# Performance work log

Measured on AMD Instinct MI355X. Metric: run time of the kernel, lower is better.

The kernel has to match this reference:

```python
import jax, jax.numpy as jnp
import numpy as np

N_NODES = 100000
N_EDGES = 200000
B_GRAPHS = 128
H = 8
DC = 256
DE = 124           # dim_embedding; node features are DE + 4 = 128
DV = 64


def setup_inputs() -> dict:
    key = jax.random.key(0)
    ks = jax.random.split(key, 10)

    def unif(k, shape):
        stdv = 1.0 / np.sqrt(shape[-1])
        return jax.random.uniform(k, shape, jnp.float32, -stdv, stdv)

    x = jax.random.normal(ks[0], (N_NODES, DE + 4), jnp.float32)
    edge_index = jax.random.randint(ks[1], (2, N_EDGES), 0, N_NODES)
    batch = jnp.sort(jax.random.randint(ks[2], (N_NODES,), 0, B_GRAPHS))
    context = jax.random.normal(ks[3], (B_GRAPHS, DC), jnp.float32)
    Wq = unif(ks[4], (H, DC, DV))
    Wk = unif(ks[5], (H, DE + 4, DV))
    Wv = unif(ks[6], (H, DE + 4, DV))
    query_coef = unif(ks[7], (1,))
    Wf = unif(ks[8], (DV, DE))
    return {"x": x, "edge_index": edge_index, "batch": batch, "context": context,
            "Wq": Wq, "Wk": Wk, "Wv": Wv, "query_coef": query_coef, "Wf": Wf}


def reference(x, edge_index, batch, context, Wq, Wk, Wv, query_coef, Wf):
    # edge_index is unused by the original forward.
    n_heads, _, dv = Wq.shape
    n_graphs = context.shape[0]

    query = jnp.einsum('bc,hcv->hbv', context, Wq)       # [H, B, Dv]
    keys = jnp.einsum('ne,hev->hnv', x, Wk)              # [H, N, Dv]
    values = jnp.einsum('ne,hev->hnv', x, Wv)            # [H, N, Dv]

    # original builds u = keys @ query^T [H,N,B] then gathers u[h,n,batch[n]];
    # compute only the gathered per-node score directly (same math).
    q_node = query[:, batch, :]                          # [H, N, Dv]
    u = jnp.sum(keys * q_node, axis=-1) / jnp.sqrt(jnp.asarray(dv, x.dtype))  # [H, N]

    # segment softmax per head over nodes of each graph
    seg_max = jax.vmap(lambda s: jax.ops.segment_max(s, batch, num_segments=n_graphs))(u)
    e = jnp.exp(u - seg_max[:, batch])                   # [H, N]
    seg_sum = jax.vmap(lambda s: jax.ops.segment_sum(s, batch, num_segments=n_graphs))(e)
    a = e / (seg_sum[:, batch] + 1e-16)                  # [H, N]

    v = a[..., None] * values                            # [H, N, Dv]
    agg = jax.vmap(lambda s: jax.ops.segment_sum(s, batch, num_segments=n_graphs))(v)  # [H, B, Dv]

    h = query_coef * query + agg                         # [H, B, Dv]
    h = jnp.einsum('hbv,ve->hbe', h, Wf)                 # [H, B, De]
    return jnp.sum(h, axis=0)                            # [B, De]
```

## Files before the change

### kernel.cpp

```cpp
#include <hip/hip_runtime.h>

#define N_NODES 100000
#define B_GRAPHS 128
#define H_HEADS 8
#define DC 256
#define DF 128
#define DV 64
#define DE 124
#define SPLITS 8
#define PART_STRIDE (H_HEADS * DF + H_HEADS)


__device__ __forceinline__ float red32(float v) {
  v += __int_as_float(__builtin_amdgcn_update_dpp(0, __float_as_int(v), 0xB1,  0xF, 0xF, true));
  v += __int_as_float(__builtin_amdgcn_update_dpp(0, __float_as_int(v), 0x4E,  0xF, 0xF, true));
  v += __int_as_float(__builtin_amdgcn_update_dpp(0, __float_as_int(v), 0x141, 0xF, 0xF, true));
  v += __int_as_float(__builtin_amdgcn_update_dpp(0, __float_as_int(v), 0x140, 0xF, 0xF, true));
  v += __int_as_float(__builtin_amdgcn_ds_swizzle(__float_as_int(v), 0x401f));
  return v;
}

__global__ __launch_bounds__(256) void k_prep(
    const float* __restrict__ context, const float* __restrict__ Wq,
    const float* __restrict__ Wk, const int* __restrict__ batch,
    float* __restrict__ query_ws, float* __restrict__ kq_ws, int* __restrict__ starts)
{
  const int b = blockIdx.x;
  const int t = threadIdx.x;
  __shared__ float ctxs[DC];
  __shared__ float qs[H_HEADS * DV];
  ctxs[t] = context[b * DC + t];
  if (t == 0) {
    int lo = 0, hi = N_NODES;
    while (lo < hi) { int m = (lo + hi) >> 1; if (batch[m] < b) lo = m + 1; else hi = m; }
    starts[b] = lo;
    if (b == 0) starts[B_GRAPHS] = N_NODES;
  }
  __syncthreads();
  for (int i = t; i < H_HEADS * DV; i += 256) {
    const int h = i >> 6, v = i & 63;
    const float* wq = Wq + (size_t)h * DC * DV + v;
    float acc = 0.f;
    for (int c = 0; c < DC; ++c) acc += ctxs[c] * wq[c * DV];
    qs[i] = acc;
    query_ws[(h * B_GRAPHS + b) * DV + v] = acc;
  }
  __syncthreads();
  for (int i = t; i < H_HEADS * DF; i += 256) {
    const int h = i >> 7, e = i & 127;
    const float4* wk = reinterpret_cast<const float4*>(Wk + ((size_t)h * DF + e) * DV);
    const float4* q4 = reinterpret_cast<const float4*>(qs + h * DV);
    float acc = 0.f;
    #pragma unroll
    for (int v4 = 0; v4 < DV / 4; ++v4) {
      const float4 a = wk[v4], q = q4[v4];
      acc += a.x * q.x + a.y * q.y + a.z * q.z + a.w * q.w;
    }
    kq_ws[(h * B_GRAPHS + b) * DF + e] = acc * 0.125f;
  }
}

__global__ __launch_bounds__(256) void k_main(
    const float* __restrict__ x, const float* __restrict__ kq_ws,
    const int* __restrict__ starts, float* __restrict__ partials)
{
  const int bid = blockIdx.x;
  const int g = bid >> 3, sp = bid & 7;
  const int t = threadIdx.x;
  const int grp = t >> 5, l32 = t & 31;
  const int s0 = starts[g], s1 = starts[g + 1];
  const int len = s1 - s0;
  const int i0 = s0 + (len * sp) / SPLITS;
  const int i1 = s0 + (len * (sp + 1)) / SPLITS;

  float4 kqr[H_HEADS];
  #pragma unroll
  for (int h = 0; h < H_HEADS; ++h)
    kqr[h] = *reinterpret_cast<const float4*>(kq_ws + (h * B_GRAPHS + g) * DF + 4 * l32);

  float4 s[H_HEADS];
  float l[H_HEADS];
  #pragma unroll
  for (int h = 0; h < H_HEADS; ++h) { s[h] = make_float4(0.f, 0.f, 0.f, 0.f); l[h] = 0.f; }

  int n = i0 + grp;
  float4 x4 = make_float4(0.f, 0.f, 0.f, 0.f);
  if (n < i1) x4 = *reinterpret_cast<const float4*>(x + (size_t)n * DF + 4 * l32);
  while (n < i1) {
    const int nn = n + 8;
    float4 xn = make_float4(0.f, 0.f, 0.f, 0.f);
    if (nn < i1) xn = *reinterpret_cast<const float4*>(x + (size_t)nn * DF + 4 * l32);
    float u[H_HEADS];
    #pragma unroll
    for (int h = 0; h < H_HEADS; ++h)
      u[h] = x4.x * kqr[h].x + x4.y * kqr[h].y + x4.z * kqr[h].z + x4.w * kqr[h].w;
    #pragma unroll
    for (int h = 0; h < H_HEADS; ++h) u[h] = red32(u[h]);
    #pragma unroll
    for (int h = 0; h < H_HEADS; ++h) {
      const float e = __expf(u[h]);
      l[h] += e;
      s[h].x += e * x4.x; s[h].y += e * x4.y; s[h].z += e * x4.z; s[h].w += e * x4.w;
    }
    x4 = xn; n = nn;
  }

  __shared__ float sbuf[8][H_HEADS][DF];
  __shared__ float lbuf[8][H_HEADS];
  #pragma unroll
  for (int h = 0; h < H_HEADS; ++h)
    *reinterpret_cast<float4*>(&sbuf[grp][h][4 * l32]) = s[h];
  if (l32 == 0) {
    #pragma unroll
    for (int h = 0; h < H_HEADS; ++h) lbuf[grp][h] = l[h];
  }
  __syncthreads();
  float* part = partials + (size_t)bid * PART_STRIDE;
  for (int i = t; i < H_HEADS * DF; i += 256) {
    const int h = i >> 7, e = i & 127;
    float acc = 0.f;
    #pragma unroll
    for (int gq = 0; gq < 8; ++gq) acc += sbuf[gq][h][e];
    part[i] = acc;
  }
  if (t < H_HEADS) {
    float acc = 0.f;
    #pragma unroll
    for (int gq = 0; gq < 8; ++gq) acc += lbuf[gq][t];
    part[H_HEADS * DF + t] = acc;
  }
}

__global__ __launch_bounds__(256) void k_final(
    const float* __restrict__ partials, const float* __restrict__ query_ws,
    const float* __restrict__ Wv, const float* __restrict__ Wf,
    const float* __restrict__ qcoef, float* __restrict__ out)
{
  const int g = blockIdx.x;
  const int t = threadIdx.x;
  __shared__ float w[H_HEADS][DF];
  __shared__ float lg[H_HEADS];
  __shared__ float Gp[4][DV];
  const float* part = partials + (size_t)g * SPLITS * PART_STRIDE;
  if (t < H_HEADS) {
    float acc = 0.f;
    for (int sp = 0; sp < SPLITS; ++sp) acc += part[sp * PART_STRIDE + H_HEADS * DF + t];
    lg[t] = acc;
  }
  __syncthreads();
  for (int i = t; i < H_HEADS * DF; i += 256) {
    float acc = 0.f;
    for (int sp = 0; sp < SPLITS; ++sp) acc += part[sp * PART_STRIDE + i];
    const int h = i >> 7;
    w[h][i & 127] = acc / (lg[h] + 1e-16f);
  }
  __syncthreads();
  const float qc = qcoef[0];
  const int v = t & 63, p = t >> 6;
  float acc = qc * (query_ws[((2 * p) * B_GRAPHS + g) * DV + v] +
                    query_ws[((2 * p + 1) * B_GRAPHS + g) * DV + v]);
  #pragma unroll
  for (int hh = 2 * p; hh <= 2 * p + 1; ++hh) {
    const float* wv = Wv + ((size_t)hh * DF) * DV + v;
    for (int e = 0; e < DF; ++e) acc += w[hh][e] * wv[e * DV];
  }
  Gp[p][v] = acc;
  __syncthreads();
  if (t < DE) {
    float o = 0.f;
    for (int v2 = 0; v2 < DV; ++v2) {
      const float Gv = Gp[0][v2] + Gp[1][v2] + Gp[2][v2] + Gp[3][v2];
      o += Gv * Wf[v2 * DE + t];
    }
    out[g * DE + t] = o;
  }
}

extern "C" void kernel_launch(void* const* d_in, const int* in_sizes, int n_in,
                              void* d_out, int out_size, void* d_ws, size_t ws_size,
                              hipStream_t stream) {
  const float* x       = (const float*)d_in[0];
  const int*   batch   = (const int*)d_in[2];
  const float* context = (const float*)d_in[3];
  const float* Wq      = (const float*)d_in[4];
  const float* Wk      = (const float*)d_in[5];
  const float* Wv      = (const float*)d_in[6];
  const float* qc      = (const float*)d_in[7];
  const float* Wf      = (const float*)d_in[8];
  float* out = (float*)d_out;

  float* ws       = (float*)d_ws;
  float* query_ws = ws;
  float* kq_ws    = ws + 65536;
  float* partials = ws + 196608;
  int*   starts   = (int*)(ws + 196608 + B_GRAPHS * SPLITS * PART_STRIDE);

  hipLaunchKernelGGL(k_prep, dim3(B_GRAPHS), dim3(256), 0, stream,
                     context, Wq, Wk, batch, query_ws, kq_ws, starts);
  hipLaunchKernelGGL(k_main, dim3(B_GRAPHS * SPLITS), dim3(256), 0, stream,
                     x, kq_ws, starts, partials);
  hipLaunchKernelGGL(k_final, dim3(B_GRAPHS), dim3(256), 0, stream,
                     partials, query_ws, Wv, Wf, qc, out);
}
```

Before: 148.0 us.

## Fuse final reduction into main kernel via last-block atomic counter

Drops the separate k_final launch. The last of the eight split blocks for each graph, detected with a threadfence and an atomic counter, now does the cross-split reduction and the Wv/Wf projection, reusing the shared buffers. It also vectorizes the query projection in k_prep with float4 loads over 128 threads. This saves one kernel launch and its gap. In exchange, some blocks run a serial tail, and correctness now depends on the counter being reset in k_prep.

```diff
diff --git a/kernel.cpp b/kernel.cpp
--- a/kernel.cpp
+++ b/kernel.cpp
@@ -23,7 +23,8 @@
 __global__ __launch_bounds__(256) void k_prep(
     const float* __restrict__ context, const float* __restrict__ Wq,
     const float* __restrict__ Wk, const int* __restrict__ batch,
-    float* __restrict__ query_ws, float* __restrict__ kq_ws, int* __restrict__ starts)
+    float* __restrict__ query_ws, float* __restrict__ kq_ws,
+    int* __restrict__ starts, int* __restrict__ cnt)
 {
   const int b = blockIdx.x;
   const int t = threadIdx.x;
@@ -34,16 +35,21 @@
     int lo = 0, hi = N_NODES;
     while (lo < hi) { int m = (lo + hi) >> 1; if (batch[m] < b) lo = m + 1; else hi = m; }
     starts[b] = lo;
+    cnt[b] = 0;
     if (b == 0) starts[B_GRAPHS] = N_NODES;
   }
   __syncthreads();
-  for (int i = t; i < H_HEADS * DV; i += 256) {
-    const int h = i >> 6, v = i & 63;
-    const float* wq = Wq + (size_t)h * DC * DV + v;
-    float acc = 0.f;
-    for (int c = 0; c < DC; ++c) acc += ctxs[c] * wq[c * DV];
-    qs[i] = acc;
-    query_ws[(h * B_GRAPHS + b) * DV + v] = acc;
+  if (t < H_HEADS * DV / 4) {
+    const int h = t >> 4, v4 = (t & 15) * 4;
+    const float4* wq = reinterpret_cast<const float4*>(Wq + (size_t)h * DC * DV + v4);
+    float4 acc = make_float4(0.f, 0.f, 0.f, 0.f);
+    for (int c = 0; c < DC; ++c) {
+      const float4 w = wq[c * (DV / 4)];
+      const float cc = ctxs[c];
+      acc.x += cc * w.x; acc.y += cc * w.y; acc.z += cc * w.z; acc.w += cc * w.w;
+    }
+    *reinterpret_cast<float4*>(qs + h * DV + v4) = acc;
+    *reinterpret_cast<float4*>(query_ws + (h * B_GRAPHS + b) * DV + v4) = acc;
   }
   __syncthreads();
   for (int i = t; i < H_HEADS * DF; i += 256) {
@@ -62,7 +68,11 @@
 
 __global__ __launch_bounds__(256) void k_main(
     const float* __restrict__ x, const float* __restrict__ kq_ws,
-    const int* __restrict__ starts, float* __restrict__ partials)
+    const int* __restrict__ starts, float* __restrict__ partials,
+    int* __restrict__ cnt,
+    const float* __restrict__ query_ws, const float* __restrict__ Wv,
+    const float* __restrict__ Wf, const float* __restrict__ qcoef,
+    float* __restrict__ out)
 {
   const int bid = blockIdx.x;
   const int g = bid >> 3, sp = bid & 7;
@@ -107,6 +117,7 @@
 
   __shared__ float sbuf[8][H_HEADS][DF];
   __shared__ float lbuf[8][H_HEADS];
+  __shared__ int amlast;
   #pragma unroll
   for (int h = 0; h < H_HEADS; ++h)
     *reinterpret_cast<float4*>(&sbuf[grp][h][4 * l32]) = s[h];
@@ -129,30 +140,27 @@
     for (int gq = 0; gq < 8; ++gq) acc += lbuf[gq][t];
     part[H_HEADS * DF + t] = acc;
   }
-}
-
-__global__ __launch_bounds__(256) void k_final(
-    const float* __restrict__ partials, const float* __restrict__ query_ws,
-    const float* __restrict__ Wv, const float* __restrict__ Wf,
-    const float* __restrict__ qcoef, float* __restrict__ out)
-{
-  const int g = blockIdx.x;
-  const int t = threadIdx.x;
-  __shared__ float w[H_HEADS][DF];
-  __shared__ float lg[H_HEADS];
-  __shared__ float Gp[4][DV];
-  const float* part = partials + (size_t)g * SPLITS * PART_STRIDE;
+
+  __threadfence();
+  if (t == 0) amlast = (atomicAdd(&cnt[g], 1) == SPLITS - 1) ? 1 : 0;
+  __syncthreads();
+  if (!amlast) return;
+  __threadfence();
+
+  float* w  = &sbuf[0][0][0];
+  float* Gp = &sbuf[2][0][0];
+  float* lg = &lbuf[0][0];
+  const float* pg = partials + (size_t)g * SPLITS * PART_STRIDE;
   if (t < H_HEADS) {
     float acc = 0.f;
-    for (int sp = 0; sp < SPLITS; ++sp) acc += part[sp * PART_STRIDE + H_HEADS * DF + t];
+    for (int spx = 0; spx < SPLITS; ++spx) acc += pg[spx * PART_STRIDE + H_HEADS * DF + t];
     lg[t] = acc;
   }
   __syncthreads();
   for (int i = t; i < H_HEADS * DF; i += 256) {
     float acc = 0.f;
-    for (int sp = 0; sp < SPLITS; ++sp) acc += part[sp * PART_STRIDE + i];
-    const int h = i >> 7;
-    w[h][i & 127] = acc / (lg[h] + 1e-16f);
+    for (int spx = 0; spx < SPLITS; ++spx) acc += pg[spx * PART_STRIDE + i];
+    w[i] = acc / (lg[i >> 7] + 1e-16f);
   }
   __syncthreads();
   const float qc = qcoef[0];
@@ -162,14 +170,15 @@
   #pragma unroll
   for (int hh = 2 * p; hh <= 2 * p + 1; ++hh) {
     const float* wv = Wv + ((size_t)hh * DF) * DV + v;
-    for (int e = 0; e < DF; ++e) acc += w[hh][e] * wv[e * DV];
-  }
-  Gp[p][v] = acc;
+    const float* wh = w + hh * DF;
+    for (int e = 0; e < DF; ++e) acc += wh[e] * wv[e * DV];
+  }
+  Gp[p * DV + v] = acc;
   __syncthreads();
   if (t < DE) {
     float o = 0.f;
     for (int v2 = 0; v2 < DV; ++v2) {
-      const float Gv = Gp[0][v2] + Gp[1][v2] + Gp[2][v2] + Gp[3][v2];
+      const float Gv = Gp[0 * DV + v2] + Gp[1 * DV + v2] + Gp[2 * DV + v2] + Gp[3 * DV + v2];
       o += Gv * Wf[v2 * DE + t];
     }
     out[g * DE + t] = o;
@@ -194,11 +203,10 @@
   float* kq_ws    = ws + 65536;
   float* partials = ws + 196608;
   int*   starts   = (int*)(ws + 196608 + B_GRAPHS * SPLITS * PART_STRIDE);
+  int*   cnt      = starts + B_GRAPHS + 1;
 
   hipLaunchKernelGGL(k_prep, dim3(B_GRAPHS), dim3(256), 0, stream,
-                     context, Wq, Wk, batch, query_ws, kq_ws, starts);
+                     context, Wq, Wk, batch, query_ws, kq_ws, starts, cnt);
   hipLaunchKernelGGL(k_main, dim3(B_GRAPHS * SPLITS), dim3(256), 0, stream,
-                     x, kq_ws, starts, partials);
-  hipLaunchKernelGGL(k_final, dim3(B_GRAPHS), dim3(256), 0, stream,
-                     partials, query_ws, Wv, Wf, qc, out);
-}
+                     x, kq_ws, starts, partials, cnt, query_ws, Wv, Wf, qc, out);
+}
```

Result: slower. 275.0 us (+85.8%).

## Fuse prep, main and final kernels into one per-graph kernel

Applied to the files above, without the earlier changes.

Merges the three launches into a single kernel with one 512-thread block per graph. Each block does its own binary search, query and key-query projection, node streaming and final projection, with shared-memory reduction replacing the global partials buffer. The node loop now prefetches two rows ahead across 16 warp groups. The cost is parallelism: only 128 blocks stream the 51 MB of x instead of 1024, which may underuse the GPU's memory bandwidth.

```diff
diff --git a/kernel.cpp b/kernel.cpp
--- a/kernel.cpp
+++ b/kernel.cpp
@@ -7,9 +7,8 @@
 #define DF 128
 #define DV 64
 #define DE 124
-#define SPLITS 8
-#define PART_STRIDE (H_HEADS * DF + H_HEADS)
-
+#define THREADS 512
+#define GROUPS 16
 
 __device__ __forceinline__ float red32(float v) {
   v += __int_as_float(__builtin_amdgcn_update_dpp(0, __float_as_int(v), 0xB1,  0xF, 0xF, true));
@@ -20,35 +19,49 @@
   return v;
 }
 
-__global__ __launch_bounds__(256) void k_prep(
+__global__ __launch_bounds__(THREADS) void k_all(
+    const float* __restrict__ x, const int* __restrict__ batch,
     const float* __restrict__ context, const float* __restrict__ Wq,
-    const float* __restrict__ Wk, const int* __restrict__ batch,
-    float* __restrict__ query_ws, float* __restrict__ kq_ws, int* __restrict__ starts)
+    const float* __restrict__ Wk, const float* __restrict__ Wv,
+    const float* __restrict__ qcoef, const float* __restrict__ Wf,
+    float* __restrict__ out)
 {
-  const int b = blockIdx.x;
+  const int g = blockIdx.x;
   const int t = threadIdx.x;
+
   __shared__ float ctxs[DC];
   __shared__ float qs[H_HEADS * DV];
-  ctxs[t] = context[b * DC + t];
-  if (t == 0) {
+  __shared__ float kqs[H_HEADS * DF];
+  __shared__ float sbuf[8][H_HEADS * DF];
+  __shared__ float lbuf[GROUPS][H_HEADS];
+  __shared__ float lg[H_HEADS];
+  __shared__ float wbuf[H_HEADS * DF];
+  __shared__ float Gpart[H_HEADS][DV];
+  __shared__ float Gv[DV];
+  __shared__ int srange[2];
+
+  if (t < 2) {
+    const int target = g + t;
     int lo = 0, hi = N_NODES;
-    while (lo < hi) { int m = (lo + hi) >> 1; if (batch[m] < b) lo = m + 1; else hi = m; }
-    starts[b] = lo;
-    if (b == 0) starts[B_GRAPHS] = N_NODES;
+    while (lo < hi) { int m = (lo + hi) >> 1; if (batch[m] < target) lo = m + 1; else hi = m; }
+    srange[t] = lo;
+  }
+  if (t < DC) ctxs[t] = context[g * DC + t];
+  __syncthreads();
+
+  {
+    const int h = t >> 6, v = t & 63;
+    const float* wq = Wq + (size_t)h * DC * DV + v;
+    float acc = 0.f;
+    #pragma unroll 4
+    for (int c = 0; c < DC; ++c) acc += ctxs[c] * wq[(size_t)c * DV];
+    qs[t] = acc;
   }
   __syncthreads();
-  for (int i = t; i < H_HEADS * DV; i += 256) {
-    const int h = i >> 6, v = i & 63;
-    const float* wq = Wq + (size_t)h * DC * DV + v;
-    float acc = 0.f;
-    for (int c = 0; c < DC; ++c) acc += ctxs[c] * wq[c * DV];
-    qs[i] = acc;
-    query_ws[(h * B_GRAPHS + b) * DV + v] = acc;
-  }
-  __syncthreads();
-  for (int i = t; i < H_HEADS * DF; i += 256) {
-    const int h = i >> 7, e = i & 127;
-    const float4* wk = reinterpret_cast<const float4*>(Wk + ((size_t)h * DF + e) * DV);
+
+  for (int i = t; i < H_HEADS * DF; i += THREADS) {
+    const int h = i >> 7;
+    const float4* wk = reinterpret_cast<const float4*>(Wk + (size_t)i * DV);
     const float4* q4 = reinterpret_cast<const float4*>(qs + h * DV);
     float acc = 0.f;
     #pragma unroll
@@ -56,122 +69,112 @@
       const float4 a = wk[v4], q = q4[v4];
       acc += a.x * q.x + a.y * q.y + a.z * q.z + a.w * q.w;
     }
-    kq_ws[(h * B_GRAPHS + b) * DF + e] = acc * 0.125f;
+    kqs[i] = acc * 0.125f;
   }
-}
+  __syncthreads();
 
-__global__ __launch_bounds__(256) void k_main(
-    const float* __restrict__ x, const float* __restrict__ kq_ws,
-    const int* __restrict__ starts, float* __restrict__ partials)
-{
-  const int bid = blockIdx.x;
-  const int g = bid >> 3, sp = bid & 7;
-  const int t = threadIdx.x;
   const int grp = t >> 5, l32 = t & 31;
-  const int s0 = starts[g], s1 = starts[g + 1];
-  const int len = s1 - s0;
-  const int i0 = s0 + (len * sp) / SPLITS;
-  const int i1 = s0 + (len * (sp + 1)) / SPLITS;
+  const int i0f = srange[0], i1 = srange[1];
 
   float4 kqr[H_HEADS];
   #pragma unroll
   for (int h = 0; h < H_HEADS; ++h)
-    kqr[h] = *reinterpret_cast<const float4*>(kq_ws + (h * B_GRAPHS + g) * DF + 4 * l32);
+    kqr[h] = *reinterpret_cast<const float4*>(kqs + h * DF + 4 * l32);
 
   float4 s[H_HEADS];
   float l[H_HEADS];
   #pragma unroll
   for (int h = 0; h < H_HEADS; ++h) { s[h] = make_float4(0.f, 0.f, 0.f, 0.f); l[h] = 0.f; }
 
-  int n = i0 + grp;
-  float4 x4 = make_float4(0.f, 0.f, 0.f, 0.f);
-  if (n < i1) x4 = *reinterpret_cast<const float4*>(x + (size_t)n * DF + 4 * l32);
+  int n = i0f + grp;
+  float4 a0 = make_float4(0.f, 0.f, 0.f, 0.f);
+  float4 a1 = make_float4(0.f, 0.f, 0.f, 0.f);
+  if (n < i1)          a0 = *reinterpret_cast<const float4*>(x + (size_t)n * DF + 4 * l32);
+  if (n + GROUPS < i1) a1 = *reinterpret_cast<const float4*>(x + (size_t)(n + GROUPS) * DF + 4 * l32);
   while (n < i1) {
-    const int nn = n + 8;
-    float4 xn = make_float4(0.f, 0.f, 0.f, 0.f);
-    if (nn < i1) xn = *reinterpret_cast<const float4*>(x + (size_t)nn * DF + 4 * l32);
+    float4 a2 = make_float4(0.f, 0.f, 0.f, 0.f);
+    if (n + 2 * GROUPS < i1)
+      a2 = *reinterpret_cast<const float4*>(x + (size_t)(n + 2 * GROUPS) * DF + 4 * l32);
     float u[H_HEADS];
     #pragma unroll
     for (int h = 0; h < H_HEADS; ++h)
-      u[h] = x4.x * kqr[h].x + x4.y * kqr[h].y + x4.z * kqr[h].z + x4.w * kqr[h].w;
+      u[h] = a0.x * kqr[h].x + a0.y * kqr[h].y + a0.z * kqr[h].z + a0.w * kqr[h].w;
     #pragma unroll
     for (int h = 0; h < H_HEADS; ++h) u[h] = red32(u[h]);
     #pragma unroll
     for (int h = 0; h < H_HEADS; ++h) {
       const float e = __expf(u[h]);
       l[h] += e;
-      s[h].x += e * x4.x; s[h].y += e * x4.y; s[h].z += e * x4.z; s[h].w += e * x4.w;
+      s[h].x += e * a0.x; s[h].y += e * a0.y; s[h].z += e * a0.z; s[h].w += e * a0.w;
     }
-    x4 = xn; n = nn;
+    a0 = a1; a1 = a2; n += GROUPS;
   }
 
-  __shared__ float sbuf[8][H_HEADS][DF];
-  __shared__ float lbuf[8][H_HEADS];
-  #pragma unroll
-  for (int h = 0; h < H_HEADS; ++h)
-    *reinterpret_cast<float4*>(&sbuf[grp][h][4 * l32]) = s[h];
-  if (l32 == 0) {
+  if (grp >= 8) {
     #pragma unroll
-    for (int h = 0; h < H_HEADS; ++h) lbuf[grp][h] = l[h];
+    for (int h = 0; h < H_HEADS; ++h)
+      *reinterpret_cast<float4*>(&sbuf[grp - 8][h * DF + 4 * l32]) = s[h];
+    if (l32 == 0) {
+      #pragma unroll
+      for (int h = 0; h < H_HEADS; ++h) lbuf[grp][h] = l[h];
+    }
   }
   __syncthreads();
-  float* part = partials + (size_t)bid * PART_STRIDE;
-  for (int i = t; i < H_HEADS * DF; i += 256) {
-    const int h = i >> 7, e = i & 127;
-    float acc = 0.f;
+  if (grp < 8) {
     #pragma unroll
-    for (int gq = 0; gq < 8; ++gq) acc += sbuf[gq][h][e];
-    part[i] = acc;
+    for (int h = 0; h < H_HEADS; ++h) {
+      const float4 o = *reinterpret_cast<const float4*>(&sbuf[grp][h * DF + 4 * l32]);
+      s[h].x += o.x; s[h].y += o.y; s[h].z += o.z; s[h].w += o.w;
+      l[h] += lbuf[grp + 8][h];
+    }
   }
+  __syncthreads();
+  if (grp < 8) {
+    #pragma unroll
+    for (int h = 0; h < H_HEADS; ++h)
+      *reinterpret_cast<float4*>(&sbuf[grp][h * DF + 4 * l32]) = s[h];
+    if (l32 == 0) {
+      #pragma unroll
+      for (int h = 0; h < H_HEADS; ++h) lbuf[grp][h] = l[h];
+    }
+  }
+  __syncthreads();
   if (t < H_HEADS) {
     float acc = 0.f;
     #pragma unroll
-    for (int gq = 0; gq < 8; ++gq) acc += lbuf[gq][t];
-    part[H_HEADS * DF + t] = acc;
-  }
-}
-
-__global__ __launch_bounds__(256) void k_final(
-    const float* __restrict__ partials, const float* __restrict__ query_ws,
-    const float* __restrict__ Wv, const float* __restrict__ Wf,
-    const float* __restrict__ qcoef, float* __restrict__ out)
-{
-  const int g = blockIdx.x;
-  const int t = threadIdx.x;
-  __shared__ float w[H_HEADS][DF];
-  __shared__ float lg[H_HEADS];
-  __shared__ float Gp[4][DV];
-  const float* part = partials + (size_t)g * SPLITS * PART_STRIDE;
-  if (t < H_HEADS) {
-    float acc = 0.f;
-    for (int sp = 0; sp < SPLITS; ++sp) acc += part[sp * PART_STRIDE + H_HEADS * DF + t];
+    for (int g8 = 0; g8 < 8; ++g8) acc += lbuf[g8][t];
     lg[t] = acc;
   }
   __syncthreads();
-  for (int i = t; i < H_HEADS * DF; i += 256) {
+  for (int i = t; i < H_HEADS * DF; i += THREADS) {
     float acc = 0.f;
-    for (int sp = 0; sp < SPLITS; ++sp) acc += part[sp * PART_STRIDE + i];
-    const int h = i >> 7;
-    w[h][i & 127] = acc / (lg[h] + 1e-16f);
+    #pragma unroll
+    for (int g8 = 0; g8 < 8; ++g8) acc += sbuf[g8][i];
+    wbuf[i] = acc / (lg[i >> 7] + 1e-16f);
   }
   __syncthreads();
+
   const float qc = qcoef[0];
-  const int v = t & 63, p = t >> 6;
-  float acc = qc * (query_ws[((2 * p) * B_GRAPHS + g) * DV + v] +
-                    query_ws[((2 * p + 1) * B_GRAPHS + g) * DV + v]);
-  #pragma unroll
-  for (int hh = 2 * p; hh <= 2 * p + 1; ++hh) {
-    const float* wv = Wv + ((size_t)hh * DF) * DV + v;
-    for (int e = 0; e < DF; ++e) acc += w[hh][e] * wv[e * DV];
+  {
+    const int h = t >> 6, v = t & 63;
+    const float* wv = Wv + (size_t)h * DF * DV + v;
+    const float* wh = wbuf + h * DF;
+    float acc = qc * qs[h * DV + v];
+    #pragma unroll 4
+    for (int e = 0; e < DF; ++e) acc += wh[e] * wv[(size_t)e * DV];
+    Gpart[h][v] = acc;
   }
-  Gp[p][v] = acc;
+  __syncthreads();
+  if (t < DV) {
+    float acc = 0.f;
+    #pragma unroll
+    for (int h = 0; h < H_HEADS; ++h) acc += Gpart[h][t];
+    Gv[t] = acc;
+  }
   __syncthreads();
   if (t < DE) {
     float o = 0.f;
-    for (int v2 = 0; v2 < DV; ++v2) {
-      const float Gv = Gp[0][v2] + Gp[1][v2] + Gp[2][v2] + Gp[3][v2];
-      o += Gv * Wf[v2 * DE + t];
-    }
+    for (int v = 0; v < DV; ++v) o += Gv[v] * Wf[v * DE + t];
     out[g * DE + t] = o;
   }
 }
@@ -188,17 +191,8 @@
   const float* qc      = (const float*)d_in[7];
   const float* Wf      = (const float*)d_in[8];
   float* out = (float*)d_out;
+  (void)d_ws; (void)ws_size;
 
-  float* ws       = (float*)d_ws;
-  float* query_ws = ws;
-  float* kq_ws    = ws + 65536;
-  float* partials = ws + 196608;
-  int*   starts   = (int*)(ws + 196608 + B_GRAPHS * SPLITS * PART_STRIDE);
-
-  hipLaunchKernelGGL(k_prep, dim3(B_GRAPHS), dim3(256), 0, stream,
-                     context, Wq, Wk, batch, query_ws, kq_ws, starts);
-  hipLaunchKernelGGL(k_main, dim3(B_GRAPHS * SPLITS), dim3(256), 0, stream,
-                     x, kq_ws, starts, partials);
-  hipLaunchKernelGGL(k_final, dim3(B_GRAPHS), dim3(256), 0, stream,
-                     partials, query_ws, Wv, Wf, qc, out);
+  hipLaunchKernelGGL(k_all, dim3(B_GRAPHS), dim3(THREADS), 0, stream,
+                     x, batch, context, Wq, Wk, Wv, qc, Wf, out);
 }
```

After: 157.6 us. 1.06x slower.
